# Kernel optimization log

Measured on AMD Instinct MI355X. Metric: run time of the kernel, lower is better.

## Reference

```python
import jax, jax.numpy as jnp
import numpy as np
from jax import lax

D_MODEL = 1024
N_HEADS = 16
KERNEL = 3
STRIDE = 1
PAD = 1
BATCH = 32
SEQ = D_MODEL  # required by the module's reshape: seq_len must equal d_model


def setup_inputs() -> dict:
    key = jax.random.key(0)
    k1, k2, k3, k4, k5, k6 = jax.random.split(key, 6)
    query_sequences = jax.random.normal(k1, (BATCH, SEQ, D_MODEL), dtype=jnp.float32)
    key_sequences = jax.random.normal(k2, (BATCH, SEQ, D_MODEL), dtype=jnp.float32)
    value_sequences = jax.random.normal(k3, (BATCH, SEQ, D_MODEL), dtype=jnp.float32)
    key_value_sequence_lengths = jax.random.randint(k4, (BATCH,), 0, SEQ).astype(jnp.int64)
    # nn.Linear(d_model, n_heads*kernel_size) params (stored as (in, out) for x @ W)
    scale = 1.0 / np.sqrt(D_MODEL)
    Wq = jax.random.uniform(k5, (D_MODEL, N_HEADS * KERNEL), minval=-scale, maxval=scale, dtype=jnp.float32)
    bq = jax.random.uniform(k6, (N_HEADS * KERNEL,), minval=-scale, maxval=scale, dtype=jnp.float32)
    return {
        "query_sequences": query_sequences,
        "key_sequences": key_sequences,
        "value_sequences": value_sequences,
        "key_value_sequence_lengths": key_value_sequence_lengths,
        "Wq": Wq,
        "bq": bq,
    }


def reference(query_sequences, key_sequences, value_sequences, key_value_sequence_lengths, Wq, bq):
    B, S, D = query_sequences.shape
    # per-batch dynamic conv kernels from queries: (B, S, H*K) -> (B*H, D, K)
    # (valid because S == D, mirroring the torch .view)
    qk = jnp.einsum('bsd,df->bsf', query_sequences, Wq) + bq
    kernels = qk.reshape(B * N_HEADS, D, KERNEL)
    # keys as a single grouped-conv input: (1, B*D, S)
    keys = jnp.transpose(key_sequences, (0, 2, 1)).reshape(1, B * D, S)
    # grouped conv1d with groups = batch_size (each group: in=D, out=N_HEADS)
    out = lax.conv_general_dilated(
        keys, kernels,
        window_strides=(STRIDE,),
        padding=[(PAD, PAD)],
        dimension_numbers=('NCH', 'OIH', 'NCH'),
        feature_group_count=B,
    )
    return out.reshape(B, N_HEADS, S)
```

## Files before the change

kernel.cpp:

```cpp
#include <hip/hip_runtime.h>
#include <hip/hip_bf16.h>
#include <stdint.h>

typedef __attribute__((ext_vector_type(8))) short bf16x8;
typedef __attribute__((ext_vector_type(4))) float f32x4;

__device__ __forceinline__ short f2bf(float x) {
    __hip_bfloat16 h = __float2bfloat16(x);
    return __builtin_bit_cast(short, h);
}

__device__ __forceinline__ bf16x8 pack8(f32x4 a, f32x4 b) {
    bf16x8 r;
    r[0] = f2bf(a[0]); r[1] = f2bf(a[1]); r[2] = f2bf(a[2]); r[3] = f2bf(a[3]);
    r[4] = f2bf(b[0]); r[5] = f2bf(b[1]); r[6] = f2bf(b[2]); r[7] = f2bf(b[3]);
    return r;
}

__global__ __launch_bounds__(256) void prep_wfrag(const float* __restrict__ Wq,
                                                  short* __restrict__ wfrag) {
    int idx = blockIdx.x * 256 + threadIdx.x;
    int j    = idx & 7;
    int lane = (idx >> 3) & 63;
    int grp  = idx >> 9;
    int nf   = grp % 3;
    int ks   = grp / 3;
    int k = ks * 32 + ((lane >> 4) << 3) + j;
    int n = nf * 16 + (lane & 15);
    wfrag[idx] = f2bf(Wq[k * 48 + n]);
}

__global__ __launch_bounds__(256) void qk_gemm(const float* __restrict__ Q,
                                               const short* __restrict__ wfrag,
                                               const float* __restrict__ bq,
                                               short* __restrict__ wgtA) {
    const int l  = threadIdx.x & 63;
    const int w  = threadIdx.x >> 6;
    const int lr = l & 15;
    const int lk = l >> 4;
    const int row0 = blockIdx.x * 64 + w * 16;

    f32x4 acc[3];
    acc[0] = (f32x4){0.f, 0.f, 0.f, 0.f};
    acc[1] = acc[0];
    acc[2] = acc[0];

    const float* qbase = Q + (size_t)(row0 + lr) * 1024 + lk * 8;

    #pragma unroll 4
    for (int ks = 0; ks < 32; ++ks) {
        const float* p = qbase + ks * 32;
        f32x4 q0 = *(const f32x4*)p;
        f32x4 q1 = *(const f32x4*)(p + 4);
        bf16x8 a = pack8(q0, q1);
        const bf16x8* wp = (const bf16x8*)(wfrag + (size_t)ks * 1536 + l * 8);
        acc[0] = __builtin_amdgcn_mfma_f32_16x16x32_bf16(a, wp[0],   acc[0], 0, 0, 0);
        acc[1] = __builtin_amdgcn_mfma_f32_16x16x32_bf16(a, wp[64],  acc[1], 0, 0, 0);
        acc[2] = __builtin_amdgcn_mfma_f32_16x16x32_bf16(a, wp[128], acc[2], 0, 0, 0);
    }

    #pragma unroll
    for (int nf = 0; nf < 3; ++nf) {
        int n = nf * 16 + lr;
        float bias = bq[n];
        int t  = n / 3;
        int kk = n - t * 3;
        #pragma unroll
        for (int r = 0; r < 4; ++r) {
            int row = row0 + lk * 4 + r;
            int b   = row >> 10;
            int h   = (row >> 6) & 15;
            int sp  = row & 63;
            int dg  = sp * 2 + (t >> 3);
            int j   = t & 7;
            wgtA[(((size_t)(b * 3 + kk) * 128 + dg) << 7) + h * 8 + j] = f2bf(acc[nf][r] + bias);
        }
    }
}

__global__ __launch_bounds__(256, 4) void conv_mfma(const float* __restrict__ Key,
                                                    const short* __restrict__ wgtA,
                                                    float* __restrict__ out) {
    __shared__ short klds[2][34][128];
    __shared__ float red[2][16][17];
    const int blk = blockIdx.x;
    const int st  = blk & 31;
    const int b   = blk >> 5;
    const int s0  = st << 5;
    const int tid = threadIdx.x;
    const int l   = tid & 63;
    const int w   = tid >> 6;
    const int lr  = l & 15;
    const int lk  = l >> 4;
    const int ss  = w & 1;
    const int dh  = w >> 1;

    const int jg = tid & 15;
    const int r  = tid >> 4;
    const int dcol = ((jg & 7) << 3) + ((jg >> 3) << 9);
    const float* keyB = Key + ((size_t)b << 20) + dcol;

    const bool g0 = (s0 - 1 + r) >= 0;
    const bool g2 = (r < 2) && (s0 + 31 + r < 1024);
    const float* p0 = keyB + (size_t)(g0 ? s0 - 1 + r : 0) * 1024;
    const float* p1 = keyB + (size_t)(s0 + 15 + r) * 1024;
    const float* p2 = keyB + (size_t)(g2 ? s0 + 31 + r : 0) * 1024;

    const int row0 = r, row1 = r + 16, row2 = r + 32;
    char* ldsB = (char*)&klds[0][0][0];

    #define STB(buf, row, v) \
        *(bf16x8*)(ldsB + ((buf) * 34 + (row)) * 256 + ((jg * 16) ^ (((row) & 7) << 4))) = (v)

    const f32x4 z4 = (f32x4){0.f, 0.f, 0.f, 0.f};
    f32x4 a0, a1, b0, b1, c0, c1;

    a0 = g0 ? p0[0] : 0.f, a0 = g0 ? *(const f32x4*)p0 : z4;
    a1 = g0 ? *(const f32x4*)(p0 + 4) : z4;
    b0 = *(const f32x4*)p1;       b1 = *(const f32x4*)(p1 + 4);
    c0 = g2 ? *(const f32x4*)p2 : z4;
    c1 = g2 ? *(const f32x4*)(p2 + 4) : z4;
    STB(0, row0, pack8(a0, a1));
    STB(0, row1, pack8(b0, b1));
    if (r < 2) STB(0, row2, pack8(c0, c1));
    a0 = g0 ? *(const f32x4*)(p0 + 64) : z4;
    a1 = g0 ? *(const f32x4*)(p0 + 68) : z4;
    b0 = *(const f32x4*)(p1 + 64);  b1 = *(const f32x4*)(p1 + 68);
    c0 = g2 ? *(const f32x4*)(p2 + 64) : z4;
    c1 = g2 ? *(const f32x4*)(p2 + 68) : z4;
    __syncthreads();

    const short* wgtW = wgtA + (((size_t)b * 384 + (dh << 6) + lk) << 7) + lr * 8;

    f32x4 acc = z4;

    #pragma unroll
    for (int t = 0; t < 8; ++t) {
        const int buf = t & 1;
        #pragma unroll
        for (int k = 0; k < 3; ++k) {
            const int row = ss * 16 + lr + k;
            const char* rb = ldsB + (buf * 34 + row) * 256;
            const int sw = ((row & 7) << 4);
            #pragma unroll
            for (int kk = 0; kk < 2; ++kk) {
                bf16x8 kv = *(const bf16x8*)(rb + ((((dh << 7) + (kk << 6) + (lk << 4))) ^ sw));
                bf16x8 a  = *(const bf16x8*)(wgtW + k * 16384 + t * 1024 + kk * 512);
                acc = __builtin_amdgcn_mfma_f32_16x16x32_bf16(a, kv, acc, 0, 0, 0);
            }
        }
        if (t < 7) {
            bf16x8 wA = pack8(a0, a1);
            bf16x8 wB = pack8(b0, b1);
            bf16x8 wC = pack8(c0, c1);
            __syncthreads();
            STB(buf ^ 1, row0, wA);
            STB(buf ^ 1, row1, wB);
            if (r < 2) STB(buf ^ 1, row2, wC);
            if (t < 6) {
                const int o = (t + 2) << 6;
                a0 = g0 ? *(const f32x4*)(p0 + o) : z4;
                a1 = g0 ? *(const f32x4*)(p0 + o + 4) : z4;
                b0 = *(const f32x4*)(p1 + o);  b1 = *(const f32x4*)(p1 + o + 4);
                c0 = g2 ? *(const f32x4*)(p2 + o) : z4;
                c1 = g2 ? *(const f32x4*)(p2 + o + 4) : z4;
            }
            __syncthreads();
        }
    }
    #undef STB

    if (dh == 1) {
        #pragma unroll
        for (int r4 = 0; r4 < 4; ++r4) red[ss][lk * 4 + r4][lr] = acc[r4];
    }
    __syncthreads();
    if (dh == 0) {
        const int s = s0 + ss * 16 + lr;
        #pragma unroll
        for (int r4 = 0; r4 < 4; ++r4) {
            int h = lk * 4 + r4;
            out[(((b << 4) + h) << 10) + s] = acc[r4] + red[ss][h][lr];
        }
    }
}

extern "C" void kernel_launch(void* const* d_in, const int* in_sizes, int n_in,
                              void* d_out, int out_size, void* d_ws, size_t ws_size,
                              hipStream_t stream) {
    const float* Q  = (const float*)d_in[0];
    const float* K  = (const float*)d_in[1];
    const float* Wq = (const float*)d_in[4];
    const float* bq = (const float*)d_in[5];
    float* outp = (float*)d_out;

    short* wfrag = (short*)d_ws;
    short* wgtA  = (short*)((char*)d_ws + 98304);

    hipLaunchKernelGGL(prep_wfrag, dim3(192),  dim3(256), 0, stream, Wq, wfrag);
    hipLaunchKernelGGL(qk_gemm,    dim3(512),  dim3(256), 0, stream, Q, wfrag, bq, wgtA);
    hipLaunchKernelGGL(conv_mfma,  dim3(1024), dim3(256), 0, stream, K, wgtA, outp);
}
```

Baseline: 65.63 us.

## Give each wave a private key tile in LDS and drop block barriers

The conv kernel now has each wave load, convert and store its own 18-row by 64-column key slice into a wave-private double-buffered LDS region, instead of all four waves sharing one 34x128 tile. Because no other wave touches a wave's buffer, the two __syncthreads per pipeline step are removed. The aim is to stop waves stalling on each other during the key-streaming loop. In exchange, the halo rows are loaded twice, LDS use grows slightly, and each lane does wider contiguous loads of 16 floats.

After: 68.86 us. 1.05x slower.

```diff
diff --git a/kernel.cpp b/kernel.cpp
--- a/kernel.cpp
+++ b/kernel.cpp
@@ -81,12 +81,11 @@
 __global__ __launch_bounds__(256, 4) void conv_mfma(const float* __restrict__ Key,
                                                     const short* __restrict__ wgtA,
                                                     float* __restrict__ out) {
-    __shared__ short klds[2][34][128];
+    __shared__ short klds[4][2][18][64];
     __shared__ float red[2][16][17];
     const int blk = blockIdx.x;
     const int st  = blk & 31;
     const int b   = blk >> 5;
-    const int s0  = st << 5;
     const int tid = threadIdx.x;
     const int l   = tid & 63;
     const int w   = tid >> 6;
@@ -94,81 +93,75 @@
     const int lk  = l >> 4;
     const int ss  = w & 1;
     const int dh  = w >> 1;
+    const int sbase = (st << 5) + (ss << 4);
 
-    const int jg = tid & 15;
-    const int r  = tid >> 4;
-    const int dcol = ((jg & 7) << 3) + ((jg >> 3) << 9);
-    const float* keyB = Key + ((size_t)b << 20) + dcol;
+    const int row16 = l >> 2;
+    const int cg    = l & 3;
+    const int rowX  = 16 + (l >> 2);
+    const int srowA = sbase - 1 + row16;
+    const int srowX = sbase + 15 + (l >> 2);
+    const bool okA  = (srowA >= 0);
+    const bool okX  = (l < 8) && (srowX < 1024);
 
-    const bool g0 = (s0 - 1 + r) >= 0;
-    const bool g2 = (r < 2) && (s0 + 31 + r < 1024);
-    const float* p0 = keyB + (size_t)(g0 ? s0 - 1 + r : 0) * 1024;
-    const float* p1 = keyB + (size_t)(s0 + 15 + r) * 1024;
-    const float* p2 = keyB + (size_t)(g2 ? s0 + 31 + r : 0) * 1024;
+    const float* keyW = Key + ((size_t)b << 20) + (dh << 9);
+    const f32x4* pA = (const f32x4*)(keyW + (size_t)(okA ? srowA : 0) * 1024 + cg * 16);
+    const f32x4* pX = (const f32x4*)(keyW + (size_t)(okX ? srowX : 0) * 1024 + cg * 16);
 
-    const int row0 = r, row1 = r + 16, row2 = r + 32;
-    char* ldsB = (char*)&klds[0][0][0];
-
-    #define STB(buf, row, v) \
-        *(bf16x8*)(ldsB + ((buf) * 34 + (row)) * 256 + ((jg * 16) ^ (((row) & 7) << 4))) = (v)
+    char* ldsW = (char*)&klds[w][0][0][0];
+    const int swzA = (row16 & 7) << 4;
+    const int swzX = (rowX & 7) << 4;
 
     const f32x4 z4 = (f32x4){0.f, 0.f, 0.f, 0.f};
-    f32x4 a0, a1, b0, b1, c0, c1;
+    f32x4 mA[4], mX[4];
 
-    a0 = g0 ? p0[0] : 0.f, a0 = g0 ? *(const f32x4*)p0 : z4;
-    a1 = g0 ? *(const f32x4*)(p0 + 4) : z4;
-    b0 = *(const f32x4*)p1;       b1 = *(const f32x4*)(p1 + 4);
-    c0 = g2 ? *(const f32x4*)p2 : z4;
-    c1 = g2 ? *(const f32x4*)(p2 + 4) : z4;
-    STB(0, row0, pack8(a0, a1));
-    STB(0, row1, pack8(b0, b1));
-    if (r < 2) STB(0, row2, pack8(c0, c1));
-    a0 = g0 ? *(const f32x4*)(p0 + 64) : z4;
-    a1 = g0 ? *(const f32x4*)(p0 + 68) : z4;
-    b0 = *(const f32x4*)(p1 + 64);  b1 = *(const f32x4*)(p1 + 68);
-    c0 = g2 ? *(const f32x4*)(p2 + 64) : z4;
-    c1 = g2 ? *(const f32x4*)(p2 + 68) : z4;
-    __syncthreads();
+    #define LOADS(t) do {                                            \
+        const int o = (t) * 16;                                      \
+        mA[0] = okA ? pA[o]     : z4;  mA[1] = okA ? pA[o + 1] : z4; \
+        mA[2] = okA ? pA[o + 2] : z4;  mA[3] = okA ? pA[o + 3] : z4; \
+        mX[0] = okX ? pX[o]     : z4;  mX[1] = okX ? pX[o + 1] : z4; \
+        mX[2] = okX ? pX[o + 2] : z4;  mX[3] = okX ? pX[o + 3] : z4; \
+    } while (0)
+
+    #define WRITES(buf) do {                                                  \
+        char* bb = ldsW + (buf) * 2304;                                       \
+        *(bf16x8*)(bb + row16 * 128 + (((cg << 5))      ^ swzA)) = pack8(mA[0], mA[1]); \
+        *(bf16x8*)(bb + row16 * 128 + (((cg << 5) + 16) ^ swzA)) = pack8(mA[2], mA[3]); \
+        if (l < 8) {                                                          \
+            *(bf16x8*)(bb + rowX * 128 + (((cg << 5))      ^ swzX)) = pack8(mX[0], mX[1]); \
+            *(bf16x8*)(bb + rowX * 128 + (((cg << 5) + 16) ^ swzX)) = pack8(mX[2], mX[3]); \
+        }                                                                     \
+    } while (0)
 
     const short* wgtW = wgtA + (((size_t)b * 384 + (dh << 6) + lk) << 7) + lr * 8;
 
     f32x4 acc = z4;
+
+    LOADS(0);
+    WRITES(0);
+    LOADS(1);
 
     #pragma unroll
     for (int t = 0; t < 8; ++t) {
         const int buf = t & 1;
         #pragma unroll
         for (int k = 0; k < 3; ++k) {
-            const int row = ss * 16 + lr + k;
-            const char* rb = ldsB + (buf * 34 + row) * 256;
-            const int sw = ((row & 7) << 4);
+            const int row = lr + k;
+            const char* rb = ldsW + buf * 2304 + row * 128;
+            const int sw = (row & 7) << 4;
             #pragma unroll
             for (int kk = 0; kk < 2; ++kk) {
-                bf16x8 kv = *(const bf16x8*)(rb + ((((dh << 7) + (kk << 6) + (lk << 4))) ^ sw));
+                bf16x8 kv = *(const bf16x8*)(rb + (((kk << 6) + (lk << 4)) ^ sw));
                 bf16x8 a  = *(const bf16x8*)(wgtW + k * 16384 + t * 1024 + kk * 512);
                 acc = __builtin_amdgcn_mfma_f32_16x16x32_bf16(a, kv, acc, 0, 0, 0);
             }
         }
         if (t < 7) {
-            bf16x8 wA = pack8(a0, a1);
-            bf16x8 wB = pack8(b0, b1);
-            bf16x8 wC = pack8(c0, c1);
-            __syncthreads();
-            STB(buf ^ 1, row0, wA);
-            STB(buf ^ 1, row1, wB);
-            if (r < 2) STB(buf ^ 1, row2, wC);
-            if (t < 6) {
-                const int o = (t + 2) << 6;
-                a0 = g0 ? *(const f32x4*)(p0 + o) : z4;
-                a1 = g0 ? *(const f32x4*)(p0 + o + 4) : z4;
-                b0 = *(const f32x4*)(p1 + o);  b1 = *(const f32x4*)(p1 + o + 4);
-                c0 = g2 ? *(const f32x4*)(p2 + o) : z4;
-                c1 = g2 ? *(const f32x4*)(p2 + o + 4) : z4;
-            }
-            __syncthreads();
+            WRITES(buf ^ 1);
+            if (t < 6) LOADS(t + 2);
         }
     }
-    #undef STB
+    #undef LOADS
+    #undef WRITES
 
     if (dh == 1) {
         #pragma unroll
@@ -176,7 +169,7 @@
     }
     __syncthreads();
     if (dh == 0) {
-        const int s = s0 + ss * 16 + lr;
+        const int s = sbase + lr;
         #pragma unroll
         for (int r4 = 0; r4 < 4; ++r4) {
             int h = lk * 4 + r4;
```
